# Performance work log

Hardware: AMD Instinct MI355X
Metric: run time of the kernel (lower is better)

## Reference

```python
import jax, jax.numpy as jnp
import numpy as np

N = 20000      # nodes
E = 320000     # edges
D = 128        # h feature dim
L = 2          # EGCL layers
MH = 256       # mlp_m hidden
MO = 128       # mlp_m output (message dim)
XH = 256       # mlp_x hidden
HH = 256       # mlp_h hidden
MIN = 2 * D + 1  # 257: cat(h_i, h_j, ||dx||^2)


def silu(z):
    return z * jax.nn.sigmoid(z)


def setup_inputs() -> dict:
    key = jax.random.key(0)
    ks = jax.random.split(key, 18)
    s = 0.05
    return {
        "edge_index": jax.random.randint(ks[0], (2, E), 0, N, dtype=jnp.int64 if jax.config.jax_enable_x64 else jnp.int32),
        "h": jax.random.normal(ks[1], (N, D), dtype=jnp.float32),
        "x": jax.random.normal(ks[2], (N, 3), dtype=jnp.float32),
        # per-layer stacked MLP params
        "Wm1": jax.random.normal(ks[3], (L, MIN, MH), dtype=jnp.float32) * s,
        "bm1": jnp.zeros((L, MH), dtype=jnp.float32),
        "Wm2": jax.random.normal(ks[4], (L, MH, MO), dtype=jnp.float32) * s,
        "bm2": jnp.zeros((L, MO), dtype=jnp.float32),
        "Wx1": jax.random.normal(ks[5], (L, MIN, XH), dtype=jnp.float32) * s,
        "bx1": jnp.zeros((L, XH), dtype=jnp.float32),
        "Wx2": jax.random.normal(ks[6], (L, XH, 3), dtype=jnp.float32) * s,
        "bx2": jnp.zeros((L, 3), dtype=jnp.float32),
        "Wh1": jax.random.normal(ks[7], (L, D + MO, HH), dtype=jnp.float32) * s,
        "bh1": jnp.zeros((L, HH), dtype=jnp.float32),
        "Wh2": jax.random.normal(ks[8], (L, HH, D), dtype=jnp.float32) * s,
        "bh2": jnp.zeros((L, D), dtype=jnp.float32),
        "Wa": jax.random.normal(ks[9], (L, MO, 1), dtype=jnp.float32) * s,
        "ba": jnp.zeros((L, 1), dtype=jnp.float32),
    }


def reference(edge_index, h, x, Wm1, bm1, Wm2, bm2, Wx1, bx1, Wx2, bx2,
              Wh1, bh1, Wh2, bh2, Wa, ba):
    # flow='target_to_source': i = edge_index[0], j = edge_index[1],
    # aggregation (scatter-sum) indexed by edge_index[0].
    src = edge_index[0]
    dst = edge_index[1]
    n_nodes = h.shape[0]
    n_layers = Wm1.shape[0]
    for l in range(n_layers):
        hi, hj = h[src], h[dst]                       # [E, D] gathers
        diff = x[src] - x[dst]                        # [E, 3]
        d2 = jnp.sum(diff * diff, axis=1, keepdims=True)  # ||dx||^2, [E, 1]
        feat = jnp.concatenate([hi, hj, d2], axis=1)  # [E, 2D+1]
        # --- h message: mlp_m + sigmoid attention gate ---
        m = silu(feat @ Wm1[l] + bm1[l]) @ Wm2[l] + bm2[l]   # [E, MO]
        m = m * jax.nn.sigmoid(m @ Wa[l] + ba[l])
        agg_h = jax.ops.segment_sum(m, src, num_segments=n_nodes)  # [N, MO]
        new_h = silu(jnp.concatenate([h, agg_h], axis=1) @ Wh1[l] + bh1[l]) @ Wh2[l] + bh2[l]
        # --- x message (uses OLD h, as in original forward) ---
        mx = silu(feat @ Wx1[l] + bx1[l]) @ Wx2[l] + bx2[l]  # [E, 3]
        # NOTE: original uses torch.norm(coords_i - coords_j) with NO dim ->
        # a single global Frobenius norm over all edges; reproduced faithfully.
        gnorm = jnp.sqrt(jnp.sum(diff * diff))
        xm = diff * mx / (gnorm + 1.0)                # [E, 3]
        new_x = x + jax.ops.segment_sum(xm, src, num_segments=n_nodes)
        h, x = new_h, new_x
    return (h, x)
```

## Files before the change

### kernel.cpp

```cpp
#include <hip/hip_runtime.h>
#include <hip/hip_bf16.h>

#define N_NODES 20000
#define N_EDGES 320000
#define D 128

typedef __attribute__((ext_vector_type(8))) short short8;
typedef __attribute__((ext_vector_type(4))) float f32x4;

__device__ __forceinline__ float sigmoid_f(float z) { return 1.f / (1.f + __expf(-z)); }
__device__ __forceinline__ float silu_f(float z) { return z * sigmoid_f(z); }
__device__ __forceinline__ short f2bf(float f) {
    union { float f; unsigned u; } a; a.f = f;
    unsigned r = a.u + 0x7fff + ((a.u >> 16) & 1);
    return (short)(r >> 16);
}
__device__ __forceinline__ float bf2f(short s) {
    union { unsigned u; float f; } a; a.u = ((unsigned)(unsigned short)s) << 16;
    return a.f;
}

__global__ void hist_kernel(const int* __restrict__ ei, int* __restrict__ hist) {
    int e = blockIdx.x * 256 + threadIdx.x;
    if (e < N_EDGES) atomicAdd(&hist[ei[e]], 1);
}

__global__ void scan_kernel(const int* __restrict__ hist, int* __restrict__ offs) {
    __shared__ int part[1024];
    __shared__ int ppre[1024];
    int t = threadIdx.x;
    int base = t * 20;
    int s = 0;
    for (int j = 0; j < 20; j++) { int i = base + j; if (i < N_NODES) s += hist[i]; }
    part[t] = s;
    __syncthreads();
    if (t == 0) { int acc = 0; for (int i = 0; i < 1024; i++) { ppre[i] = acc; acc += part[i]; } }
    __syncthreads();
    int run = ppre[t];
    for (int j = 0; j < 20; j++) {
        int i = base + j;
        if (i < N_NODES) { offs[i] = run; run += hist[i]; }
    }
}

__global__ void scatter_kernel(const int* __restrict__ ei, const int* __restrict__ offs,
                               int* __restrict__ cursor,
                               int* __restrict__ es, int* __restrict__ ed) {
    int e = blockIdx.x * 256 + threadIdx.x;
    if (e < N_EDGES) {
        int s = ei[e], d = ei[N_EDGES + e];
        int p = offs[s] + atomicAdd(&cursor[s], 1);
        es[p] = s; ed[p] = d;
    }
}

__global__ void precompute_kernel(const int* __restrict__ es, const int* __restrict__ ed,
                                  const float* __restrict__ x,
                                  float* __restrict__ gsum) {
    int e = blockIdx.x * blockDim.x + threadIdx.x;
    float local = 0.f;
    if (e < N_EDGES) {
        int s = es[e];
        int d = ed[e];
        float dx = x[s * 3 + 0] - x[d * 3 + 0];
        float dy = x[s * 3 + 1] - x[d * 3 + 1];
        float dz = x[s * 3 + 2] - x[d * 3 + 2];
        local = dx * dx + dy * dy + dz * dz;
    }
    #pragma unroll
    for (int o = 32; o > 0; o >>= 1) local += __shfl_down(local, o, 64);
    if ((threadIdx.x & 63) == 0) atomicAdd(gsum, local);
}

__global__ void prep_weights(const float* __restrict__ Wm1, const float* __restrict__ Wx1,
                             const float* __restrict__ Wm2, const float* __restrict__ Wh1,
                             const float* __restrict__ Wh2, const float* __restrict__ Wx2,
                             short* __restrict__ WcatT, short* __restrict__ Wm2T,
                             short* __restrict__ Wh1T, short* __restrict__ Wh2T,
                             short* __restrict__ Wx2T) {
    int idx = blockIdx.x * 256 + threadIdx.x;
    if (idx < 131072) {
        int seg = idx >> 15, r = idx & 32767, k = r >> 8, c = r & 255;
        const float* s = (seg == 0) ? Wm1 : (seg == 1) ? Wx1
                        : (seg == 2) ? Wm1 + 128 * 256 : Wx1 + 128 * 256;
        WcatT[(size_t)(seg * 256 + c) * 128 + k] = f2bf(s[k * 256 + c]);
    } else if (idx < 163840) {
        int r = idx - 131072, k = r >> 7, c = r & 127;
        Wm2T[c * 256 + k] = f2bf(Wm2[k * 128 + c]);
    } else if (idx < 229376) {
        int r = idx - 163840, k = r >> 8, c = r & 255;
        Wh1T[c * 256 + k] = f2bf(Wh1[k * 256 + c]);
    } else if (idx < 262144) {
        int r = idx - 229376, k = r >> 7, c = r & 127;
        Wh2T[c * 256 + k] = f2bf(Wh2[k * 128 + c]);
    } else {
        int r = idx - 262144, c = r >> 8, k = r & 255;
        Wx2T[c * 256 + k] = (c < 3) ? f2bf(Wx2[k * 3 + c]) : (short)0;
    }
}

__global__ __launch_bounds__(256, 4) void tgemm_kernel(const float* __restrict__ h,
        const short* __restrict__ WcatT, short* __restrict__ T) {
    int tid = threadIdx.x, w = tid >> 6, l = tid & 63;
    int l15 = l & 15, kg = l >> 4;
    int rowbase = blockIdx.x * 64 + w * 16;
    int cg = blockIdx.y;
    int arow = rowbase + l15; if (arow >= N_NODES) arow = N_NODES - 1;
    f32x4 acc[16];
    #pragma unroll
    for (int ct = 0; ct < 16; ct++) acc[ct] = (f32x4){0.f, 0.f, 0.f, 0.f};
    #pragma unroll
    for (int ks = 0; ks < 4; ks++) {
        int kb = ks * 32 + kg * 8;
        const f32x4* hp = (const f32x4*)(h + (size_t)arow * 128 + kb);
        f32x4 h0 = hp[0], h1 = hp[1];
        short8 a;
        a[0] = f2bf(h0.x); a[1] = f2bf(h0.y); a[2] = f2bf(h0.z); a[3] = f2bf(h0.w);
        a[4] = f2bf(h1.x); a[5] = f2bf(h1.y); a[6] = f2bf(h1.z); a[7] = f2bf(h1.w);
        #pragma unroll
        for (int ct = 0; ct < 16; ct++) {
            short8 b = *(const short8*)(WcatT + (size_t)(cg * 256 + ct * 16 + l15) * 128 + kb);
            acc[ct] = __builtin_amdgcn_mfma_f32_16x16x32_bf16(a, b, acc[ct], 0, 0, 0);
        }
    }
    #pragma unroll
    for (int ct = 0; ct < 16; ct++) {
        #pragma unroll
        for (int r = 0; r < 4; r++) {
            int node = rowbase + kg * 4 + r;
            if (node < N_NODES)
                T[(size_t)node * 1024 + cg * 256 + ct * 16 + l15] = f2bf(acc[ct][r]);
        }
    }
}

__global__ __launch_bounds__(256, 6) void edge_kernel(
    const int* __restrict__ es, const int* __restrict__ ed,
    const short* __restrict__ T, const float* __restrict__ xc,
    const float* __restrict__ gsum,
    const float* __restrict__ Wm1r, const float* __restrict__ bm1,
    const short* __restrict__ Wm2T, const float* __restrict__ bm2,
    const float* __restrict__ Wa, const float* __restrict__ ba,
    const float* __restrict__ Wx1r, const float* __restrict__ bx1,
    const short* __restrict__ Wx2T, const float* __restrict__ bx2,
    float* __restrict__ agg_h, float* __restrict__ aggx) {
    __shared__ float sdiff[64][4];
    int tid = threadIdx.x, w = tid >> 6, l = tid & 63;
    int l15 = l & 15, kg = l >> 4;
    int ebase = blockIdx.x * 64 + w * 16;
    int e = ebase + l15;
    int src = es[e], dst = ed[e];
    float dfx = xc[src * 3 + 0] - xc[dst * 3 + 0];
    float dfy = xc[src * 3 + 1] - xc[dst * 3 + 1];
    float dfz = xc[src * 3 + 2] - xc[dst * 3 + 2];
    float d2v = dfx * dfx + dfy * dfy + dfz * dfz;
    if (kg == 0) {
        sdiff[w * 16 + l15][0] = dfx;
        sdiff[w * 16 + l15][1] = dfy;
        sdiff[w * 16 + l15][2] = dfz;
    }
    __syncthreads();

    int srow[4];
    #pragma unroll
    for (int r = 0; r < 4; r++) srow[r] = es[ebase + kg * 4 + r];

    f32x4 acc[8];
    #pragma unroll
    for (int ct = 0; ct < 8; ct++) { float bv = bm2[ct * 16 + l15]; acc[ct] = (f32x4){bv, bv, bv, bv}; }
    #pragma unroll
    for (int ks = 0; ks < 8; ks++) {
        int cb = ks * 32 + kg * 8;
        short8 ts = *(const short8*)(T + (size_t)src * 1024 + cb);
        short8 td = *(const short8*)(T + (size_t)dst * 1024 + 512 + cb);
        f32x4 w0 = ((const f32x4*)(Wm1r + cb))[0], w1 = ((const f32x4*)(Wm1r + cb))[1];
        f32x4 b0 = ((const f32x4*)(bm1 + cb))[0], b1 = ((const f32x4*)(bm1 + cb))[1];
        float wv[8], bv[8];
        *(f32x4*)&wv[0] = w0; *(f32x4*)&wv[4] = w1;
        *(f32x4*)&bv[0] = b0; *(f32x4*)&bv[4] = b1;
        short8 a;
        #pragma unroll
        for (int i = 0; i < 8; i++) {
            float z = bf2f(ts[i]) + bf2f(td[i]) + d2v * wv[i] + bv[i];
            a[i] = f2bf(silu_f(z));
        }
        #pragma unroll
        for (int ct = 0; ct < 8; ct++) {
            short8 b = *(const short8*)(Wm2T + (size_t)(ct * 16 + l15) * 256 + cb);
            acc[ct] = __builtin_amdgcn_mfma_f32_16x16x32_bf16(a, b, acc[ct], 0, 0, 0);
        }
    }
    float part[4] = {0.f, 0.f, 0.f, 0.f};
    #pragma unroll
    for (int ct = 0; ct < 8; ct++) {
        float wa = Wa[ct * 16 + l15];
        #pragma unroll
        for (int r = 0; r < 4; r++) part[r] += acc[ct][r] * wa;
    }
    #pragma unroll
    for (int m = 1; m < 16; m <<= 1) {
        #pragma unroll
        for (int r = 0; r < 4; r++) part[r] += __shfl_xor(part[r], m, 64);
    }
    float ba0 = ba[0];
    float gate[4];
    #pragma unroll
    for (int r = 0; r < 4; r++) gate[r] = sigmoid_f(part[r] + ba0);
    #pragma unroll
    for (int ct = 0; ct < 8; ct++) {
        int c = ct * 16 + l15;
        float run = acc[ct][0] * gate[0];
        #pragma unroll
        for (int r = 1; r < 4; r++) {
            float v = acc[ct][r] * gate[r];
            if (srow[r] == srow[r - 1]) {
                run += v;
            } else {
                atomicAdd(&agg_h[(size_t)srow[r - 1] * 128 + c], run);
                run = v;
            }
        }
        atomicAdd(&agg_h[(size_t)srow[3] * 128 + c], run);
    }

    float bxi = (l15 < 3) ? bx2[l15] : 0.f;
    f32x4 accx = (f32x4){bxi, bxi, bxi, bxi};
    #pragma unroll
    for (int ks = 0; ks < 8; ks++) {
        int cb = ks * 32 + kg * 8;
        short8 ts = *(const short8*)(T + (size_t)src * 1024 + 256 + cb);
        short8 td = *(const short8*)(T + (size_t)dst * 1024 + 768 + cb);
        f32x4 w0 = ((const f32x4*)(Wx1r + cb))[0], w1 = ((const f32x4*)(Wx1r + cb))[1];
        f32x4 b0 = ((const f32x4*)(bx1 + cb))[0], b1 = ((const f32x4*)(bx1 + cb))[1];
        float wv[8], bv[8];
        *(f32x4*)&wv[0] = w0; *(f32x4*)&wv[4] = w1;
        *(f32x4*)&bv[0] = b0; *(f32x4*)&bv[4] = b1;
        short8 a;
        #pragma unroll
        for (int i = 0; i < 8; i++) {
            float z = bf2f(ts[i]) + bf2f(td[i]) + d2v * wv[i] + bv[i];
            a[i] = f2bf(silu_f(z));
        }
        short8 b = *(const short8*)(Wx2T + (size_t)l15 * 256 + cb);
        accx = __builtin_amdgcn_mfma_f32_16x16x32_bf16(a, b, accx, 0, 0, 0);
    }
    if (l15 < 3) {
        float gn = sqrtf(gsum[0]);
        float invg = 1.f / (gn + 1.f);
        #pragma unroll
        for (int r = 0; r < 4; r++) {
            float df = sdiff[w * 16 + kg * 4 + r][l15];
            atomicAdd(&aggx[(size_t)srow[r] * 3 + l15], df * accx[r] * invg);
        }
    }
}

__global__ __launch_bounds__(256, 4) void node_kernel(
    const float* __restrict__ hc, const float* __restrict__ xc,
    const float* __restrict__ agg_h, const float* __restrict__ aggx,
    const short* __restrict__ Wh1T, const float* __restrict__ bh1,
    const short* __restrict__ Wh2T, const float* __restrict__ bh2,
    float* __restrict__ ho, float* __restrict__ xo) {
    __shared__ short sH[64][264];
    int tid = threadIdx.x, w = tid >> 6, l = tid & 63;
    int l15 = l & 15, kg = l >> 4;
    int nbase = blockIdx.x * 64;
    int arow = nbase + w * 16 + l15;
    int arc = (arow < N_NODES) ? arow : (N_NODES - 1);

    f32x4 acc1[16];
    #pragma unroll
    for (int ct = 0; ct < 16; ct++) { float bv = bh1[ct * 16 + l15]; acc1[ct] = (f32x4){bv, bv, bv, bv}; }
    #pragma unroll
    for (int ks = 0; ks < 8; ks++) {
        int kb = ks * 32 + kg * 8;
        const float* sp = (kb < 128) ? (hc + (size_t)arc * 128 + kb)
                                     : (agg_h + (size_t)arc * 128 + (kb - 128));
        f32x4 h0 = ((const f32x4*)sp)[0], h1 = ((const f32x4*)sp)[1];
        short8 a;
        a[0] = f2bf(h0.x); a[1] = f2bf(h0.y); a[2] = f2bf(h0.z); a[3] = f2bf(h0.w);
        a[4] = f2bf(h1.x); a[5] = f2bf(h1.y); a[6] = f2bf(h1.z); a[7] = f2bf(h1.w);
        #pragma unroll
        for (int ct = 0; ct < 16; ct++) {
            short8 b = *(const short8*)(Wh1T + (size_t)(ct * 16 + l15) * 256 + kb);
            acc1[ct] = __builtin_amdgcn_mfma_f32_16x16x32_bf16(a, b, acc1[ct], 0, 0, 0);
        }
    }
    #pragma unroll
    for (int ct = 0; ct < 16; ct++)
        #pragma unroll
        for (int r = 0; r < 4; r++)
            sH[w * 16 + kg * 4 + r][ct * 16 + l15] = f2bf(silu_f(acc1[ct][r]));
    __syncthreads();

    f32x4 acc2[8];
    #pragma unroll
    for (int ct = 0; ct < 8; ct++) { float bv = bh2[ct * 16 + l15]; acc2[ct] = (f32x4){bv, bv, bv, bv}; }
    #pragma unroll
    for (int ks = 0; ks < 8; ks++) {
        int kb = ks * 32 + kg * 8;
        short8 a = *(const short8*)&sH[w * 16 + l15][kb];
        #pragma unroll
        for (int ct = 0; ct < 8; ct++) {
            short8 b = *(const short8*)(Wh2T + (size_t)(ct * 16 + l15) * 256 + kb);
            acc2[ct] = __builtin_amdgcn_mfma_f32_16x16x32_bf16(a, b, acc2[ct], 0, 0, 0);
        }
    }
    #pragma unroll
    for (int ct = 0; ct < 8; ct++)
        #pragma unroll
        for (int r = 0; r < 4; r++) {
            int node = nbase + w * 16 + kg * 4 + r;
            if (node < N_NODES) ho[(size_t)node * 128 + ct * 16 + l15] = acc2[ct][r];
        }

    if (tid < 192) {
        int nn = tid / 3, c = tid - nn * 3;
        int node = nbase + nn;
        if (node < N_NODES)
            xo[(size_t)node * 3 + c] = xc[(size_t)node * 3 + c] + aggx[(size_t)node * 3 + c];
    }
}

extern "C" void kernel_launch(void* const* d_in, const int* in_sizes, int n_in,
                              void* d_out, int out_size, void* d_ws, size_t ws_size,
                              hipStream_t stream) {
    const int* ei = (const int*)d_in[0];
    const float* h_in = (const float*)d_in[1];
    const float* x_in = (const float*)d_in[2];
    const float* Wm1 = (const float*)d_in[3];
    const float* bm1 = (const float*)d_in[4];
    const float* Wm2 = (const float*)d_in[5];
    const float* bm2 = (const float*)d_in[6];
    const float* Wx1 = (const float*)d_in[7];
    const float* bx1 = (const float*)d_in[8];
    const float* Wx2 = (const float*)d_in[9];
    const float* bx2 = (const float*)d_in[10];
    const float* Wh1 = (const float*)d_in[11];
    const float* bh1 = (const float*)d_in[12];
    const float* Wh2 = (const float*)d_in[13];
    const float* bh2 = (const float*)d_in[14];
    const float* Wa = (const float*)d_in[15];
    const float* ba = (const float*)d_in[16];

    char* wsb = (char*)d_ws;
    short* T      = (short*)wsb;  wsb += (size_t)N_NODES * 1024 * 2;
    short* WcatT  = (short*)wsb;  wsb += (size_t)1024 * 128 * 2;
    short* Wm2T   = (short*)wsb;  wsb += (size_t)128 * 256 * 2;
    short* Wh1T   = (short*)wsb;  wsb += (size_t)256 * 256 * 2;
    short* Wh2T   = (short*)wsb;  wsb += (size_t)128 * 256 * 2;
    short* Wx2T   = (short*)wsb;  wsb += (size_t)16 * 256 * 2;
    float* agg_h  = (float*)wsb;  wsb += (size_t)N_NODES * 128 * 4;
    float* aggx   = (float*)wsb;  wsb += (size_t)N_NODES * 3 * 4;
    int*   es     = (int*)wsb;    wsb += (size_t)N_EDGES * 4;
    int*   ed     = (int*)wsb;    wsb += (size_t)N_EDGES * 4;
    int*   hist   = (int*)wsb;    wsb += (size_t)N_NODES * 4;
    int*   cursor = (int*)wsb;    wsb += (size_t)N_NODES * 4;
    float* gsum   = (float*)wsb;  wsb += 16;
    int*   offs   = (int*)wsb;    wsb += (size_t)(N_NODES + 16) * 4;

    float* h_out_f = (float*)d_out;
    float* x_out_f = h_out_f + (size_t)N_NODES * D;

    hipMemsetAsync(hist, 0, sizeof(int) * N_NODES, stream);
    hipMemsetAsync(cursor, 0, sizeof(int) * N_NODES, stream);
    hist_kernel<<<(N_EDGES + 255) / 256, 256, 0, stream>>>(ei, hist);
    scan_kernel<<<1, 1024, 0, stream>>>(hist, offs);
    scatter_kernel<<<(N_EDGES + 255) / 256, 256, 0, stream>>>(ei, offs, cursor, es, ed);

    for (int l = 0; l < 2; l++) {
        const float* hc = (l == 0) ? h_in : h_out_f;
        const float* xc = (l == 0) ? x_in : x_out_f;
        float* ho = h_out_f;
        float* xo = x_out_f;

        const float* Wm1_l = Wm1 + (size_t)l * 257 * 256;
        const float* Wx1_l = Wx1 + (size_t)l * 257 * 256;

        hipMemsetAsync(gsum, 0, sizeof(float), stream);
        hipMemsetAsync(agg_h, 0, sizeof(float) * (size_t)N_NODES * 128, stream);
        hipMemsetAsync(aggx, 0, sizeof(float) * (size_t)N_NODES * 3, stream);

        prep_weights<<<1040, 256, 0, stream>>>(
            Wm1_l, Wx1_l, Wm2 + (size_t)l * 256 * 128,
            Wh1 + (size_t)l * 256 * 256, Wh2 + (size_t)l * 256 * 128,
            Wx2 + (size_t)l * 256 * 3,
            WcatT, Wm2T, Wh1T, Wh2T, Wx2T);

        precompute_kernel<<<(N_EDGES + 255) / 256, 256, 0, stream>>>(es, ed, xc, gsum);

        tgemm_kernel<<<dim3((N_NODES + 63) / 64, 4), 256, 0, stream>>>(hc, WcatT, T);

        edge_kernel<<<N_EDGES / 64, 256, 0, stream>>>(
            es, ed, T, xc, gsum,
            Wm1_l + 256 * 256, bm1 + (size_t)l * 256,
            Wm2T, bm2 + (size_t)l * 128,
            Wa + (size_t)l * 128, ba + l,
            Wx1_l + 256 * 256, bx1 + (size_t)l * 256,
            Wx2T, bx2 + (size_t)l * 3,
            agg_h, aggx);

        node_kernel<<<(N_NODES + 63) / 64, 256, 0, stream>>>(
            hc, xc, agg_h, aggx,
            Wh1T, bh1 + (size_t)l * 256,
            Wh2T, bh2 + (size_t)l * 128,
            ho, xo);
    }
}
```

Before: 1.155 ms.

## Stage destination-node T rows in swizzled LDS with coalesced loads, merge memsets

Result: no change. 1.157 ms (+0.1%).

```diff
diff --git a/kernel.cpp b/kernel.cpp
--- a/kernel.cpp
+++ b/kernel.cpp
@@ -134,7 +134,7 @@
     }
 }
 
-__global__ __launch_bounds__(256, 6) void edge_kernel(
+__global__ __launch_bounds__(256, 5) void edge_kernel(
     const int* __restrict__ es, const int* __restrict__ ed,
     const short* __restrict__ T, const float* __restrict__ xc,
     const float* __restrict__ gsum,
@@ -144,20 +144,28 @@
     const float* __restrict__ Wx1r, const float* __restrict__ bx1,
     const short* __restrict__ Wx2T, const float* __restrict__ bx2,
     float* __restrict__ agg_h, float* __restrict__ aggx) {
-    __shared__ float sdiff[64][4];
+    __shared__ short8 sTD[64][32];
     int tid = threadIdx.x, w = tid >> 6, l = tid & 63;
     int l15 = l & 15, kg = l >> 4;
-    int ebase = blockIdx.x * 64 + w * 16;
+    int e0 = blockIdx.x * 64;
+    int ebase = e0 + w * 16;
     int e = ebase + l15;
     int src = es[e], dst = ed[e];
+    int row = w * 16 + l15;
     float dfx = xc[src * 3 + 0] - xc[dst * 3 + 0];
     float dfy = xc[src * 3 + 1] - xc[dst * 3 + 1];
     float dfz = xc[src * 3 + 2] - xc[dst * 3 + 2];
     float d2v = dfx * dfx + dfy * dfy + dfz * dfz;
-    if (kg == 0) {
-        sdiff[w * 16 + l15][0] = dfx;
-        sdiff[w * 16 + l15][1] = dfy;
-        sdiff[w * 16 + l15][2] = dfz;
+
+    int el = tid >> 2, p = tid & 3;
+    int drow = ed[e0 + el];
+    {
+        const short8* gp = (const short8*)(T + (size_t)drow * 1024 + 512 + p * 64);
+        #pragma unroll
+        for (int j = 0; j < 8; j++) {
+            int slot = p * 8 + j;
+            sTD[el][(slot & ~7) | ((slot ^ el) & 7)] = gp[j];
+        }
     }
     __syncthreads();
 
@@ -172,7 +180,8 @@
     for (int ks = 0; ks < 8; ks++) {
         int cb = ks * 32 + kg * 8;
         short8 ts = *(const short8*)(T + (size_t)src * 1024 + cb);
-        short8 td = *(const short8*)(T + (size_t)dst * 1024 + 512 + cb);
+        int slot = ks * 4 + kg;
+        short8 td = sTD[row][(slot & ~7) | ((slot ^ row) & 7)];
         f32x4 w0 = ((const f32x4*)(Wm1r + cb))[0], w1 = ((const f32x4*)(Wm1r + cb))[1];
         f32x4 b0 = ((const f32x4*)(bm1 + cb))[0], b1 = ((const f32x4*)(bm1 + cb))[1];
         float wv[8], bv[8];
@@ -223,13 +232,25 @@
         atomicAdd(&agg_h[(size_t)srow[3] * 128 + c], run);
     }
 
+    __syncthreads();
+    {
+        const short8* gp = (const short8*)(T + (size_t)drow * 1024 + 768 + p * 64);
+        #pragma unroll
+        for (int j = 0; j < 8; j++) {
+            int slot = p * 8 + j;
+            sTD[el][(slot & ~7) | ((slot ^ el) & 7)] = gp[j];
+        }
+    }
+    __syncthreads();
+
     float bxi = (l15 < 3) ? bx2[l15] : 0.f;
     f32x4 accx = (f32x4){bxi, bxi, bxi, bxi};
     #pragma unroll
     for (int ks = 0; ks < 8; ks++) {
         int cb = ks * 32 + kg * 8;
         short8 ts = *(const short8*)(T + (size_t)src * 1024 + 256 + cb);
-        short8 td = *(const short8*)(T + (size_t)dst * 1024 + 768 + cb);
+        int slot = ks * 4 + kg;
+        short8 td = sTD[row][(slot & ~7) | ((slot ^ row) & 7)];
         f32x4 w0 = ((const f32x4*)(Wx1r + cb))[0], w1 = ((const f32x4*)(Wx1r + cb))[1];
         f32x4 b0 = ((const f32x4*)(bx1 + cb))[0], b1 = ((const f32x4*)(bx1 + cb))[1];
         float wv[8], bv[8];
@@ -249,7 +270,10 @@
         float invg = 1.f / (gn + 1.f);
         #pragma unroll
         for (int r = 0; r < 4; r++) {
-            float df = sdiff[w * 16 + kg * 4 + r][l15];
+            int lsrc = kg * 4 + r;
+            float df = (l15 == 0) ? __shfl(dfx, lsrc, 64)
+                     : (l15 == 1) ? __shfl(dfy, lsrc, 64)
+                                  : __shfl(dfz, lsrc, 64);
             atomicAdd(&aggx[(size_t)srow[r] * 3 + l15], df * accx[r] * invg);
         }
     }
@@ -352,18 +376,17 @@
     short* Wx2T   = (short*)wsb;  wsb += (size_t)16 * 256 * 2;
     float* agg_h  = (float*)wsb;  wsb += (size_t)N_NODES * 128 * 4;
     float* aggx   = (float*)wsb;  wsb += (size_t)N_NODES * 3 * 4;
+    float* gsum   = (float*)wsb;  wsb += 16;
     int*   es     = (int*)wsb;    wsb += (size_t)N_EDGES * 4;
     int*   ed     = (int*)wsb;    wsb += (size_t)N_EDGES * 4;
     int*   hist   = (int*)wsb;    wsb += (size_t)N_NODES * 4;
     int*   cursor = (int*)wsb;    wsb += (size_t)N_NODES * 4;
-    float* gsum   = (float*)wsb;  wsb += 16;
     int*   offs   = (int*)wsb;    wsb += (size_t)(N_NODES + 16) * 4;
 
     float* h_out_f = (float*)d_out;
     float* x_out_f = h_out_f + (size_t)N_NODES * D;
 
-    hipMemsetAsync(hist, 0, sizeof(int) * N_NODES, stream);
-    hipMemsetAsync(cursor, 0, sizeof(int) * N_NODES, stream);
+    hipMemsetAsync(hist, 0, sizeof(int) * N_NODES * 2, stream);
     hist_kernel<<<(N_EDGES + 255) / 256, 256, 0, stream>>>(ei, hist);
     scan_kernel<<<1, 1024, 0, stream>>>(hist, offs);
     scatter_kernel<<<(N_EDGES + 255) / 256, 256, 0, stream>>>(ei, offs, cursor, es, ed);
@@ -377,9 +400,9 @@
         const float* Wm1_l = Wm1 + (size_t)l * 257 * 256;
         const float* Wx1_l = Wx1 + (size_t)l * 257 * 256;
 
-        hipMemsetAsync(gsum, 0, sizeof(float), stream);
-        hipMemsetAsync(agg_h, 0, sizeof(float) * (size_t)N_NODES * 128, stream);
-        hipMemsetAsync(aggx, 0, sizeof(float) * (size_t)N_NODES * 3, stream);
+        hipMemsetAsync(agg_h, 0,
+                       sizeof(float) * ((size_t)N_NODES * 128 + (size_t)N_NODES * 3) + 16,
+                       stream);
 
         prep_weights<<<1040, 256, 0, stream>>>(
             Wm1_l, Wx1_l, Wm2 + (size_t)l * 256 * 128,
```
